# Optimization experiments

Hardware: AMD Instinct MI355X
Metric: run time of the kernel (lower is better)

Reference implementation:

```python
import jax, jax.numpy as jnp
import numpy as np

GROUPS = 32
EPS = 1e-5


def setup_inputs() -> dict:
    key = jax.random.key(0)
    ks = jax.random.split(key, 6)
    B, H, W, C = 2, 64, 64, 512
    wscale = 0.02  # keep logits in a sane range for softmax
    return {
        "x": jax.random.normal(ks[0], (B, H, W, C), dtype=jnp.float32),
        "gamma": jnp.ones((C,), jnp.float32),
        "beta": jnp.zeros((C,), jnp.float32),
        "wq": jax.random.normal(ks[1], (C, C), dtype=jnp.float32) * wscale,
        "bq": jnp.zeros((C,), jnp.float32),
        "wk": jax.random.normal(ks[2], (C, C), dtype=jnp.float32) * wscale,
        "bk": jnp.zeros((C,), jnp.float32),
        "wv": jax.random.normal(ks[3], (C, C), dtype=jnp.float32) * wscale,
        "bv": jnp.zeros((C,), jnp.float32),
        "wp": jax.random.normal(ks[4], (C, C), dtype=jnp.float32) * wscale,
        "bp": jnp.zeros((C,), jnp.float32),
    }


def _group_norm(x, gamma, beta):
    B, H, W, C = x.shape
    xg = x.reshape(B, H, W, GROUPS, C // GROUPS)
    mean = xg.mean(axis=(1, 2, 4), keepdims=True)
    var = xg.var(axis=(1, 2, 4), keepdims=True)
    xn = ((xg - mean) * jax.lax.rsqrt(var + EPS)).reshape(B, H, W, C)
    return xn * gamma + beta


def reference(x, gamma, beta, wq, bq, wk, bk, wv, bv, wp, bp):
    B, H, W, C = x.shape
    xn = _group_norm(x, gamma, beta)
    # 1x1 convs == per-pixel linear layers
    q = (xn @ wq + bq).reshape(B, H * W, C)
    k = (xn @ wk + bk).reshape(B, H * W, C)
    v = (xn @ wv + bv).reshape(B, H * W, C)
    scale = C ** (-0.5)
    attn = jax.nn.softmax(jnp.einsum("bqc,bkc->bqk", q, k) * scale, axis=-1)
    out = jnp.einsum("bqk,bkc->bqc", attn, v).reshape(B, H, W, C)
    return (out @ wp + bp) + x
```

## Files before the change

### kernel.cpp

```cpp
#include <hip/hip_runtime.h>


typedef __bf16 bf16_t;
typedef __bf16 bf16x8 __attribute__((ext_vector_type(8)));
typedef __bf16 bf16x4 __attribute__((ext_vector_type(4)));
typedef float  f32x4  __attribute__((ext_vector_type(4)));

__device__ __forceinline__ bf16x8 ld8(const bf16_t* p) {
    return *reinterpret_cast<const bf16x8*>(p);
}
__device__ __forceinline__ f32x4 mfma16(bf16x8 a, bf16x8 b, f32x4 c) {
    return __builtin_amdgcn_mfma_f32_16x16x32_bf16(a, b, c, 0, 0, 0);
}
__device__ __forceinline__ void gload16(const bf16_t* gp, bf16_t* lp) {
    __builtin_amdgcn_global_load_lds(
        (const __attribute__((address_space(1))) void*)gp,
        (__attribute__((address_space(3))) void*)lp, 16, 0, 0);
}

#define NPIX 8192
#define C512 512
#define SEQ  4096
#define QSCALE 0.044194173824159216f

__global__ __launch_bounds__(256) void gn_stats_k(const float* __restrict__ x,
                                                  float* __restrict__ stats) {
    int bg = blockIdx.x;
    int b  = bg >> 5, g = bg & 31;
    const float* xp = x + (size_t)b * SEQ * C512 + g * 16;
    float s = 0.f, s2 = 0.f;
    for (int p = threadIdx.x; p < SEQ; p += 256) {
        const float4* q = reinterpret_cast<const float4*>(xp + (size_t)p * C512);
        #pragma unroll
        for (int i = 0; i < 4; i++) {
            float4 v = q[i];
            s  += v.x + v.y + v.z + v.w;
            s2 += v.x*v.x + v.y*v.y + v.z*v.z + v.w*v.w;
        }
    }
    #pragma unroll
    for (int off = 32; off >= 1; off >>= 1) {
        s  += __shfl_down(s, off);
        s2 += __shfl_down(s2, off);
    }
    __shared__ float rs[4], rs2[4];
    int wave = threadIdx.x >> 6;
    if ((threadIdx.x & 63) == 0) { rs[wave] = s; rs2[wave] = s2; }
    __syncthreads();
    if (threadIdx.x == 0) {
        float S = 0.f, S2 = 0.f;
        for (int i = 0; i < 4; i++) { S += rs[i]; S2 += rs2[i]; }
        float mean = S * (1.f / 65536.f);
        float var  = S2 * (1.f / 65536.f) - mean * mean;
        stats[bg * 2]     = mean;
        stats[bg * 2 + 1] = rsqrtf(var + 1e-5f);
    }
}

__global__ __launch_bounds__(256) void wt_conv_k(const float* wq, const float* wk,
                                                 const float* wv, const float* wp,
                                                 bf16_t* wqkvT, bf16_t* wpT) {
    int y = blockIdx.y;
    const float* w = (y == 0) ? wq : (y == 1) ? wk : (y == 2) ? wv : wp;
    float scale = (y == 0) ? QSCALE : 1.0f;
    int tid = blockIdx.x * 256 + threadIdx.x;
    int n = tid >> 9, k = tid & 511;
    bf16_t val = (bf16_t)(w[(size_t)k * C512 + n] * scale);
    if (y < 3) wqkvT[((size_t)y * C512 + n) * C512 + k] = val;
    else       wpT[(size_t)n * C512 + k] = val;
}

__global__ __launch_bounds__(256) void bias_merge_k(const float* bq, const float* bk,
                                                    const float* bv, float* bqkv) {
    int i = blockIdx.x * 256 + threadIdx.x;
    float v = (i < 512) ? bq[i] * QSCALE : (i < 1024) ? bk[i - 512] : bv[i - 1024];
    bqkv[i] = v;
}

__global__ __launch_bounds__(256) void xn_k(const float* __restrict__ x,
                                            const float* __restrict__ stats,
                                            const float* __restrict__ gamma,
                                            const float* __restrict__ beta,
                                            bf16_t* __restrict__ xn) {
    size_t idx = ((size_t)blockIdx.x * 256 + threadIdx.x) * 4;
    int c = (int)(idx & 511);
    size_t pix = idx >> 9;
    int b = (int)(pix >> 12);
    int g = c >> 4;
    float mean = stats[(b * 32 + g) * 2];
    float rstd = stats[(b * 32 + g) * 2 + 1];
    float4 v  = *reinterpret_cast<const float4*>(x + idx);
    float4 gm = *reinterpret_cast<const float4*>(gamma + c);
    float4 bt = *reinterpret_cast<const float4*>(beta + c);
    bf16x4 o;
    o[0] = (bf16_t)((v.x - mean) * rstd * gm.x + bt.x);
    o[1] = (bf16_t)((v.y - mean) * rstd * gm.y + bt.y);
    o[2] = (bf16_t)((v.z - mean) * rstd * gm.z + bt.z);
    o[3] = (bf16_t)((v.w - mean) * rstd * gm.w + bt.w);
    *reinterpret_cast<bf16x4*>(xn + idx) = o;
}

template <int MODE>
__global__ __launch_bounds__(256, 2) void gemm128_k(
        const bf16_t* __restrict__ Aall, const bf16_t* __restrict__ Ball,
        const float* __restrict__ bias, const float* __restrict__ resid,
        void* __restrict__ out0, void* __restrict__ out1,
        void* __restrict__ out2) {
    __shared__ bf16_t as_[2][4096];
    __shared__ bf16_t bs_[2][4096];

    int lane = threadIdx.x & 63;
    int w    = threadIdx.x >> 6;
    int wr   = w >> 1, wc = w & 1;
    int lrow = lane & 15, quad = lane >> 4;
    int bz   = blockIdx.z;

    const bf16_t* A;
    const bf16_t* B;
    size_t lda, ldb;
    int ksteps;
    if (MODE == 0)      { A = Aall;                         B = Ball;                        lda = 512;  ldb = 512;  ksteps = 16;  }
    else if (MODE == 1) { A = Aall + (size_t)bz*SEQ*C512;   B = Ball + (size_t)bz*SEQ*C512;  lda = 512;  ldb = 512;  ksteps = 16;  }
    else if (MODE == 2) { A = Aall + (size_t)bz*SEQ*SEQ;    B = Ball + (size_t)bz*C512*SEQ;  lda = SEQ;  ldb = SEQ;  ksteps = 128; }
    else                { A = Aall;                         B = Ball;                        lda = 512;  ldb = 512;  ksteps = 16;  }

    int bm = blockIdx.x * 128, bn = blockIdx.y * 128;

    auto stage = [&](int buf, int ks) {
        size_t k0 = (size_t)ks * 32;
        #pragma unroll
        for (int ii = 0; ii < 2; ii++) {
            int c = w * 2 + ii;
            const bf16_t* gpA = A + (size_t)(bm + c * 16 + lrow) * lda + k0 + quad * 8;
            gload16(gpA, &as_[buf][c * 512]);
            const bf16_t* gpB = B + (size_t)(bn + c * 16 + lrow) * ldb + k0 + quad * 8;
            gload16(gpB, &bs_[buf][c * 512]);
        }
    };

    f32x4 acc[4][4] = {};
    f32x4 lacc[4] = {};
    bf16x8 onesf;
    #pragma unroll
    for (int j = 0; j < 8; j++) onesf[j] = (bf16_t)1.0f;

    stage(0, 0);

    for (int ks = 0; ks < ksteps; ks++) {
        int cur = ks & 1;
        __syncthreads();
        if (ks + 1 < ksteps) stage(1 - cur, ks + 1);

        const bf16_t* al = &as_[cur][(wr * 4) * 512];
        const bf16_t* bl = &bs_[cur][(wc * 4) * 512];
        bf16x8 af[4], bf[4];
        #pragma unroll
        for (int m = 0; m < 4; m++) af[m] = ld8(al + m * 512 + lane * 8);
        #pragma unroll
        for (int n = 0; n < 4; n++) bf[n] = ld8(bl + n * 512 + lane * 8);
        #pragma unroll
        for (int m = 0; m < 4; m++)
            #pragma unroll
            for (int n = 0; n < 4; n++)
                acc[m][n] = mfma16(af[m], bf[n], acc[m][n]);
        if (MODE == 2) {
            #pragma unroll
            for (int m = 0; m < 4; m++) lacc[m] = mfma16(af[m], onesf, lacc[m]);
        }
    }

    #pragma unroll
    for (int m = 0; m < 4; m++) {
        int rowb = bm + wr * 64 + m * 16 + quad * 4;
        #pragma unroll
        for (int n = 0; n < 4; n++) {
            int col = bn + wc * 64 + n * 16 + lrow;
            #pragma unroll
            for (int i = 0; i < 4; i++) {
                int row = rowb + i;
                float v = acc[m][n][i];
                if (MODE == 0) {
                    int seg = col >> 9, c = col & 511;
                    bf16_t val = (bf16_t)(v + bias[col]);
                    if (seg == 0) {
                        ((bf16_t*)out0)[(size_t)row * C512 + c] = val;
                    } else if (seg == 1) {
                        ((bf16_t*)out1)[(size_t)row * C512 + c] = val;
                    } else {
                        int b = row >> 12, s = row & 4095;
                        ((bf16_t*)out2)[((size_t)(b * C512 + c)) * SEQ + s] = val;
                    }
                } else if (MODE == 1) {
                    bf16_t* P = (bf16_t*)out0 + (size_t)bz * SEQ * SEQ;
                    P[(size_t)row * SEQ + col] = (bf16_t)__expf(fminf(v, 20.0f));
                } else if (MODE == 2) {
                    float o = v / lacc[m][i];
                    ((bf16_t*)out0)[((size_t)bz * SEQ + row) * C512 + col] = (bf16_t)o;
                } else {
                    size_t idx = (size_t)row * C512 + col;
                    ((float*)out0)[idx] = v + bias[col] + resid[idx];
                }
            }
        }
    }
}

extern "C" void kernel_launch(void* const* d_in, const int* in_sizes, int n_in,
                              void* d_out, int out_size, void* d_ws, size_t ws_size,
                              hipStream_t stream) {
    const float* x     = (const float*)d_in[0];
    const float* gamma = (const float*)d_in[1];
    const float* beta  = (const float*)d_in[2];
    const float* wq = (const float*)d_in[3];  const float* bq = (const float*)d_in[4];
    const float* wk = (const float*)d_in[5];  const float* bk = (const float*)d_in[6];
    const float* wv = (const float*)d_in[7];  const float* bv = (const float*)d_in[8];
    const float* wp = (const float*)d_in[9];  const float* bp = (const float*)d_in[10];
    float* out = (float*)d_out;

    char* ws = (char*)d_ws;
    size_t off = 0;
    float*  stats  = (float*)(ws + off);   off += 1024;
    float*  bqkv   = (float*)(ws + off);   off += 1536 * sizeof(float);
    bf16_t* xn     = (bf16_t*)(ws + off);  off += (size_t)NPIX * C512 * 2;
    bf16_t* wqkvT  = (bf16_t*)(ws + off);  off += (size_t)3 * C512 * C512 * 2;
    bf16_t* wpT    = (bf16_t*)(ws + off);  off += (size_t)C512 * C512 * 2;
    bf16_t* Qb     = (bf16_t*)(ws + off);  off += (size_t)NPIX * C512 * 2;
    bf16_t* Kb     = (bf16_t*)(ws + off);  off += (size_t)NPIX * C512 * 2;
    bf16_t* VTb    = (bf16_t*)(ws + off);  off += (size_t)NPIX * C512 * 2;
    bf16_t* P      = (bf16_t*)(ws + off);  off += (size_t)2 * SEQ * SEQ * 2;
    bf16_t* Ob = xn;

    gn_stats_k<<<64, 256, 0, stream>>>(x, stats);
    wt_conv_k<<<dim3(1024, 4), 256, 0, stream>>>(wq, wk, wv, wp, wqkvT, wpT);
    bias_merge_k<<<6, 256, 0, stream>>>(bq, bk, bv, bqkv);
    xn_k<<<4096, 256, 0, stream>>>(x, stats, gamma, beta, xn);

    gemm128_k<0><<<dim3(64, 12, 1), 256, 0, stream>>>(
        xn, wqkvT, bqkv, nullptr, Qb, Kb, VTb);

    gemm128_k<1><<<dim3(32, 32, 2), 256, 0, stream>>>(
        Qb, Kb, nullptr, nullptr, P, nullptr, nullptr);

    gemm128_k<2><<<dim3(32, 4, 2), 256, 0, stream>>>(
        P, VTb, nullptr, nullptr, Ob, nullptr, nullptr);

    gemm128_k<3><<<dim3(64, 4, 1), 256, 0, stream>>>(
        Ob, wpT, bp, x, out, nullptr, nullptr);
}
```

Measured before the change: 357.3 us.

## Split-K the P·V GEMM four ways and move softmax row sums into QK epilogue

The attention-times-V GEMM is split along the key dimension into four partial GEMMs writing separate bf16 buffers, so four times as many blocks run. The softmax row sums are now accumulated with atomics in the QK^T exp epilogue instead of an extra MFMA against a ones vector. A new combine kernel sums the partials and divides by the row sum. The change adds workspace traffic for the partials, a memset and an extra launch, and rounds the partials to bf16 before they are summed.

```diff
diff --git a/kernel.cpp b/kernel.cpp
--- a/kernel.cpp
+++ b/kernel.cpp
@@ -105,7 +105,8 @@
         const bf16_t* __restrict__ Aall, const bf16_t* __restrict__ Ball,
         const float* __restrict__ bias, const float* __restrict__ resid,
         void* __restrict__ out0, void* __restrict__ out1,
-        void* __restrict__ out2) {
+        void* __restrict__ out2, void* __restrict__ out3,
+        float* __restrict__ lsum) {
     __shared__ bf16_t as_[2][4096];
     __shared__ bf16_t bs_[2][4096];
 
@@ -118,16 +119,17 @@
     const bf16_t* A;
     const bf16_t* B;
     size_t lda, ldb;
-    int ksteps;
-    if (MODE == 0)      { A = Aall;                         B = Ball;                        lda = 512;  ldb = 512;  ksteps = 16;  }
-    else if (MODE == 1) { A = Aall + (size_t)bz*SEQ*C512;   B = Ball + (size_t)bz*SEQ*C512;  lda = 512;  ldb = 512;  ksteps = 16;  }
-    else if (MODE == 2) { A = Aall + (size_t)bz*SEQ*SEQ;    B = Ball + (size_t)bz*C512*SEQ;  lda = SEQ;  ldb = SEQ;  ksteps = 128; }
-    else                { A = Aall;                         B = Ball;                        lda = 512;  ldb = 512;  ksteps = 16;  }
+    int ksteps, kofs = 0, zb = bz, sp = 0;
+    if (MODE == 0)      { A = Aall;                         B = Ball;                        lda = 512;  ldb = 512;  ksteps = 16; }
+    else if (MODE == 1) { A = Aall + (size_t)bz*SEQ*C512;   B = Ball + (size_t)bz*SEQ*C512;  lda = 512;  ldb = 512;  ksteps = 16; }
+    else if (MODE == 2) { zb = bz >> 2; sp = bz & 3;
+                          A = Aall + (size_t)zb*SEQ*SEQ;    B = Ball + (size_t)zb*C512*SEQ;  lda = SEQ;  ldb = SEQ;  ksteps = 32; kofs = sp * 1024; }
+    else                { A = Aall;                         B = Ball;                        lda = 512;  ldb = 512;  ksteps = 16; }
 
     int bm = blockIdx.x * 128, bn = blockIdx.y * 128;
 
     auto stage = [&](int buf, int ks) {
-        size_t k0 = (size_t)ks * 32;
+        size_t k0 = (size_t)kofs + (size_t)ks * 32;
         #pragma unroll
         for (int ii = 0; ii < 2; ii++) {
             int c = w * 2 + ii;
@@ -139,10 +141,6 @@
     };
 
     f32x4 acc[4][4] = {};
-    f32x4 lacc[4] = {};
-    bf16x8 onesf;
-    #pragma unroll
-    for (int j = 0; j < 8; j++) onesf[j] = (bf16_t)1.0f;
 
     stage(0, 0);
 
@@ -163,10 +161,14 @@
             #pragma unroll
             for (int n = 0; n < 4; n++)
                 acc[m][n] = mfma16(af[m], bf[n], acc[m][n]);
-        if (MODE == 2) {
+    }
+
+    float rs[4][4];
+    if (MODE == 1) {
+        #pragma unroll
+        for (int m = 0; m < 4; m++)
             #pragma unroll
-            for (int m = 0; m < 4; m++) lacc[m] = mfma16(af[m], onesf, lacc[m]);
-        }
+            for (int i = 0; i < 4; i++) rs[m][i] = 0.f;
     }
 
     #pragma unroll
@@ -191,11 +193,14 @@
                         ((bf16_t*)out2)[((size_t)(b * C512 + c)) * SEQ + s] = val;
                     }
                 } else if (MODE == 1) {
+                    float p = __expf(fminf(v, 20.0f));
                     bf16_t* P = (bf16_t*)out0 + (size_t)bz * SEQ * SEQ;
-                    P[(size_t)row * SEQ + col] = (bf16_t)__expf(fminf(v, 20.0f));
+                    P[(size_t)row * SEQ + col] = (bf16_t)p;
+                    rs[m][i] += p;
                 } else if (MODE == 2) {
-                    float o = v / lacc[m][i];
-                    ((bf16_t*)out0)[((size_t)bz * SEQ + row) * C512 + col] = (bf16_t)o;
+                    bf16_t* Ops = (bf16_t*)((sp == 0) ? out0 : (sp == 1) ? out1
+                                          : (sp == 2) ? out2 : out3);
+                    Ops[((size_t)zb * SEQ + row) * C512 + col] = (bf16_t)v;
                 } else {
                     size_t idx = (size_t)row * C512 + col;
                     ((float*)out0)[idx] = v + bias[col] + resid[idx];
@@ -203,6 +208,45 @@
             }
         }
     }
+
+    if (MODE == 1) {
+        #pragma unroll
+        for (int m = 0; m < 4; m++) {
+            #pragma unroll
+            for (int i = 0; i < 4; i++) {
+                float r = rs[m][i];
+                r += __shfl_xor(r, 1);
+                r += __shfl_xor(r, 2);
+                r += __shfl_xor(r, 4);
+                r += __shfl_xor(r, 8);
+                if (lrow == 0) {
+                    int row = bm + wr * 64 + m * 16 + quad * 4 + i;
+                    atomicAdd(&lsum[(size_t)bz * SEQ + row], r);
+                }
+            }
+        }
+    }
+}
+
+__global__ __launch_bounds__(256) void attn_combine_k(const bf16_t* __restrict__ Op0,
+                                                      const bf16_t* __restrict__ Op1,
+                                                      const bf16_t* __restrict__ Op2,
+                                                      const bf16_t* __restrict__ Op3,
+                                                      const float* __restrict__ lsum,
+                                                      bf16_t* __restrict__ O) {
+    int idx = blockIdx.x * 256 + threadIdx.x;
+    int row = idx >> 6;
+    int c8  = (idx & 63) << 3;
+    float inv = 1.0f / lsum[row];
+    size_t base = (size_t)row * C512 + c8;
+    bf16x8 o0 = ld8(Op0 + base), o1 = ld8(Op1 + base);
+    bf16x8 o2 = ld8(Op2 + base), o3 = ld8(Op3 + base);
+    bf16x8 o;
+    #pragma unroll
+    for (int j = 0; j < 8; j++)
+        o[j] = (bf16_t)(((float)o0[j] + (float)o1[j] +
+                         (float)o2[j] + (float)o3[j]) * inv);
+    *reinterpret_cast<bf16x8*>(O + base) = o;
 }
 
 extern "C" void kernel_launch(void* const* d_in, const int* in_sizes, int n_in,
@@ -221,14 +265,21 @@
     size_t off = 0;
     float*  stats  = (float*)(ws + off);   off += 1024;
     float*  bqkv   = (float*)(ws + off);   off += 1536 * sizeof(float);
+    float*  lsum   = (float*)(ws + off);   off += (size_t)NPIX * sizeof(float);
     bf16_t* xn     = (bf16_t*)(ws + off);  off += (size_t)NPIX * C512 * 2;
     bf16_t* wqkvT  = (bf16_t*)(ws + off);  off += (size_t)3 * C512 * C512 * 2;
     bf16_t* wpT    = (bf16_t*)(ws + off);  off += (size_t)C512 * C512 * 2;
     bf16_t* Qb     = (bf16_t*)(ws + off);  off += (size_t)NPIX * C512 * 2;
     bf16_t* Kb     = (bf16_t*)(ws + off);  off += (size_t)NPIX * C512 * 2;
     bf16_t* VTb    = (bf16_t*)(ws + off);  off += (size_t)NPIX * C512 * 2;
+    bf16_t* Op2    = (bf16_t*)(ws + off);  off += (size_t)NPIX * C512 * 2;
+    bf16_t* Op3    = (bf16_t*)(ws + off);  off += (size_t)NPIX * C512 * 2;
     bf16_t* P      = (bf16_t*)(ws + off);  off += (size_t)2 * SEQ * SEQ * 2;
-    bf16_t* Ob = xn;
+    bf16_t* Ob  = xn;
+    bf16_t* Op0 = Qb;
+    bf16_t* Op1 = Kb;
+
+    hipMemsetAsync(lsum, 0, (size_t)NPIX * sizeof(float), stream);
 
     gn_stats_k<<<64, 256, 0, stream>>>(x, stats);
     wt_conv_k<<<dim3(1024, 4), 256, 0, stream>>>(wq, wk, wv, wp, wqkvT, wpT);
@@ -236,14 +287,16 @@
     xn_k<<<4096, 256, 0, stream>>>(x, stats, gamma, beta, xn);
 
     gemm128_k<0><<<dim3(64, 12, 1), 256, 0, stream>>>(
-        xn, wqkvT, bqkv, nullptr, Qb, Kb, VTb);
+        xn, wqkvT, bqkv, nullptr, Qb, Kb, VTb, nullptr, nullptr);
 
     gemm128_k<1><<<dim3(32, 32, 2), 256, 0, stream>>>(
-        Qb, Kb, nullptr, nullptr, P, nullptr, nullptr);
-
-    gemm128_k<2><<<dim3(32, 4, 2), 256, 0, stream>>>(
-        P, VTb, nullptr, nullptr, Ob, nullptr, nullptr);
+        Qb, Kb, nullptr, nullptr, P, nullptr, nullptr, nullptr, lsum);
+
+    gemm128_k<2><<<dim3(32, 4, 8), 256, 0, stream>>>(
+        P, VTb, nullptr, nullptr, Op0, Op1, Op2, Op3, nullptr);
+
+    attn_combine_k<<<2048, 256, 0, stream>>>(Op0, Op1, Op2, Op3, lsum, Ob);
 
     gemm128_k<3><<<dim3(64, 4, 1), 256, 0, stream>>>(
-        Ob, wpT, bp, x, out, nullptr, nullptr);
-}
+        Ob, wpT, bp, x, out, nullptr, nullptr, nullptr, nullptr);
+}
```

Result: faster. 320.5 us (-10.3%).
